# Kernel optimization log

Measured on AMD Instinct MI355X. Metric: run time of the kernel, lower is better.

## Reference

```python
import jax, jax.numpy as jnp
import numpy as np

B, N, D, DEG = 64, 128, 64, 16  # graphs, nodes/graph, emb_dim, degree


def setup_inputs() -> dict:
    key = jax.random.key(0)
    k1, k2 = jax.random.split(key)
    # ring-lattice edges per graph: node i -> (i+k) % N, k=1..DEG (no self loops, no duplicates)
    src_local = jnp.repeat(jnp.arange(N, dtype=jnp.int32), DEG)            # [N*DEG]
    dst_local = (src_local + jnp.tile(jnp.arange(1, DEG + 1, dtype=jnp.int32), N)) % N
    offsets = (jnp.arange(B, dtype=jnp.int32) * N)[:, None]                 # [B,1]
    src = (src_local[None, :] + offsets).reshape(-1)                        # [B*N*DEG]
    dst = (dst_local[None, :] + offsets).reshape(-1)
    edge_index = jnp.stack([src, dst], axis=0)                              # [2, E]
    batch_vec = jnp.repeat(jnp.arange(B, dtype=jnp.int32), N)               # [B*N]
    edge_attr = jax.random.normal(k1, (B * N * DEG, D), dtype=jnp.float32)
    emb_table = jax.random.normal(k2, (3, D), dtype=jnp.float32)
    emb_table = emb_table.at[0].set(0.0)  # padding_idx=0 -> zero row
    return {"edge_attr": edge_attr, "emb_table": emb_table,
            "edge_index": edge_index, "batch_vec": batch_vec,
            "num_graphs": B, "max_nodes": N}


def reference(edge_attr, emb_table, edge_index, batch_vec, num_graphs, max_nodes):
    total_nodes = batch_vec.shape[0]
    ones = jnp.ones((total_nodes,), dtype=jnp.int32)
    counts = jax.ops.segment_sum(ones, batch_vec, num_segments=num_graphs)  # nodes per graph
    offsets = jnp.cumsum(counts) - counts                                   # exclusive cumsum
    local = jnp.arange(total_nodes, dtype=jnp.int32) - offsets[batch_vec]   # node idx within graph

    g = batch_vec[edge_index[0]]            # graph id per edge
    si = local[edge_index[0]]
    di = local[edge_index[1]]

    # to_dense_adj(edge_index, batch, edge_attr): scatter-add edge features -> [B, N, N, D]
    edge_dense = jnp.zeros((num_graphs, max_nodes, max_nodes, edge_attr.shape[-1]),
                           dtype=edge_attr.dtype)
    edge_dense = edge_dense.at[g, si, di].add(edge_attr)

    # A = 2 - dense(edge val 2, self-loop val 1, else 0) -> 0 edge, 1 diag, 2 disconnected/pad
    A = jnp.full((num_graphs, max_nodes, max_nodes), 2, dtype=jnp.int32)
    A = A.at[g, si, di].add(-2)
    A = A.at[batch_vec, local, local].add(-1)

    # Embedding(3, D, padding_idx=0): row 0 is zeros
    emb = emb_table[A] * (A != 0)[..., None].astype(emb_table.dtype)
    return edge_dense + emb
```

## Files before the change

kernel.cpp:

```cpp
#include <hip/hip_runtime.h>


typedef float f4 __attribute__((ext_vector_type(4)));


__global__ __launch_bounds__(256) void fill_u_kernel(
        f4* __restrict__ out, const f4* __restrict__ emb,
        long long total4, int D4, int lg, int lgN) {
    long long base0 = ((long long)blockIdx.x << 11) + threadIdx.x;
    long long stride = (long long)gridDim.x << 11;
    int d4 = (int)base0 & (D4 - 1);
    f4 v1 = emb[D4 + d4];
    f4 v2 = emb[2 * D4 + d4];
    int Nm1 = (1 << lgN) - 1;
    for (long long base = base0; base < total4; base += stride) {
#pragma unroll
        for (int k = 0; k < 8; ++k) {
            long long u = base + (long long)(k << 8);
            long long c = u >> lg;
            int j = (int)c & Nm1;
            int i = (int)(c >> lgN) & Nm1;
            out[u] = (j == i) ? v1 : v2;
        }
    }
}

__global__ __launch_bounds__(256) void edge_u_kernel(
        const f4* __restrict__ attr, const int* __restrict__ eidx,
        f4* __restrict__ out, int E, int N, int D4, int lg) {
    long long idx = (long long)blockIdx.x * 256 + threadIdx.x;
    if (idx < ((long long)E << lg)) {
        int e  = (int)(idx >> lg);
        int d4 = (int)idx & (D4 - 1);
        int s = eidx[e];
        int d = eidx[E + e];
        int dj = d & (N - 1);
        out[(((size_t)s * N + dj) << lg) + d4] = attr[((size_t)e << lg) + d4];
    }
}


__global__ __launch_bounds__(256) void fillprep_kernel(
        f4* __restrict__ out, const f4* __restrict__ emb,
        const int* __restrict__ batch, int* __restrict__ offs,
        int TN, int B, int D4, int fillBlocks) {
    if ((int)blockIdx.x == fillBlocks) {
        __shared__ int cnt[1024];
        for (int i = threadIdx.x; i < B; i += 256) cnt[i] = 0;
        __syncthreads();
        for (int v = threadIdx.x; v < TN; v += 256)
            atomicAdd(&cnt[batch[v]], 1);
        __syncthreads();
        if (threadIdx.x == 0) {
            int acc = 0;
            for (int g = 0; g < B; ++g) { offs[g] = acc; acc += cnt[g]; }
            offs[B] = acc;
        }
        return;
    }
    size_t base = ((size_t)blockIdx.x << 10) + threadIdx.x;
    f4 v2 = emb[2 * D4 + (int)(base & (D4 - 1))];
#pragma unroll
    for (int k = 0; k < 4; ++k)
        out[base + (size_t)k * 256] = v2;
}

__global__ __launch_bounds__(256) void diagedge_kernel(
        const f4* __restrict__ attr, const f4* __restrict__ emb,
        const int* __restrict__ eidx, const int* __restrict__ batch,
        const int* __restrict__ offs, f4* __restrict__ out,
        int E, int N, int TN, int D4, int lg) {
    long long idx = (long long)blockIdx.x * 256 + threadIdx.x;
    long long dUnits = (long long)TN << lg;
    if (idx < dUnits) {
        int n  = (int)(idx >> lg);
        int d4 = (int)idx & (D4 - 1);
        int g = batch[n];
        int i = n - offs[g];
        size_t row = (size_t)(g * N + i);
        out[(row * N + i) * D4 + d4] = emb[D4 + d4];
        return;
    }
    idx -= dUnits;
    if (idx < ((long long)E << lg)) {
        int e  = (int)(idx >> lg);
        int d4 = (int)idx & (D4 - 1);
        int s = eidx[e], d = eidx[E + e];
        int g = batch[s];
        int off = offs[g];
        size_t row = (size_t)(g * N + (s - off));
        out[(row * N + (d - off)) * D4 + d4] = attr[((size_t)e << lg) + d4];
    }
}


__global__ void prep_kernel(const int* __restrict__ batch, int* __restrict__ ws,
                            int TN, int B) {
    extern __shared__ int cnt[];
    for (int i = threadIdx.x; i < B; i += blockDim.x) cnt[i] = 0;
    __syncthreads();
    for (int v = threadIdx.x; v < TN; v += blockDim.x)
        atomicAdd(&cnt[batch[v]], 1);
    __syncthreads();
    if (threadIdx.x == 0) {
        int acc = 0;
        for (int g = 0; g < B; ++g) {
            int c = cnt[g];
            ws[g] = acc; ws[B + g] = c; acc += c;
        }
    }
}

__global__ void fill_kernel(f4* __restrict__ out, const f4* __restrict__ emb,
                            const int* __restrict__ counts, int N, int D4, int jPer) {
    int g  = blockIdx.z;
    int i  = blockIdx.y;
    int d4 = threadIdx.x % D4;
    int jj = threadIdx.x / D4;
    int j  = blockIdx.x * jPer + jj;
    if (j >= N) return;
    f4 v1 = emb[D4 + d4];
    f4 v2 = emb[2 * D4 + d4];
    bool diag = (j == i) && (i < counts[g]);
    f4 v = diag ? v1 : v2;
    size_t row = (size_t)(g * N + i);
    out[(row * N + j) * D4 + d4] = v;
}

__global__ void edge_kernel(const f4* __restrict__ attr, const int* __restrict__ eidx,
                            const int* __restrict__ batch, const int* __restrict__ offs,
                            f4* __restrict__ out, int E, int N, int D4) {
    int idx = blockIdx.x * blockDim.x + threadIdx.x;
    if (idx >= E * D4) return;
    int e  = idx / D4;
    int d4 = idx - e * D4;
    int s  = eidx[e];
    int d  = eidx[E + e];
    int g  = batch[s];
    int off = offs[g];
    out[(((size_t)g * N + (s - off)) * N + (d - off)) * D4 + d4] =
        attr[(size_t)e * D4 + d4];
}

extern "C" void kernel_launch(void* const* d_in, const int* in_sizes, int n_in,
                              void* d_out, int out_size, void* d_ws, size_t ws_size,
                              hipStream_t stream) {
    const float* edge_attr  = (const float*)d_in[0];
    const float* emb_table  = (const float*)d_in[1];
    const int*   edge_index = (const int*)d_in[2];
    const int*   batch_vec  = (const int*)d_in[3];

    int D  = in_sizes[1] / 3;
    int E  = in_sizes[2] / 2;
    int TN = in_sizes[3];
    int D4 = D / 4;
    int N  = (int)((long long)out_size / ((long long)TN * (long long)D));
    int B  = TN / N;

    f4*  out = (f4*)d_out;
    int* ws  = (int*)d_ws;

    auto ispow2 = [](int x) { return x > 0 && (x & (x - 1)) == 0; };
    long long total4 = (long long)out_size / 4;
    bool pow2D4 = ispow2(D4) && D4 <= 256 && (D % 4 == 0);
    int lg = 0; while ((1 << lg) < D4) ++lg;
    int lgN = 0; while ((1 << lgN) < N) ++lgN;

    bool uniform = pow2D4 && ispow2(N) && ((long long)B * N == TN) &&
                   (total4 % 2048 == 0);

    if (uniform) {
        long long chunks = total4 >> 11;
        int fgrid = (int)(chunks < 2048 ? chunks : 2048);
        fill_u_kernel<<<fgrid, 256, 0, stream>>>(out, (const f4*)emb_table,
                                                 total4, D4, lg, lgN);

        long long eUnits = (long long)E << lg;
        int bBlocks = (int)((eUnits + 255) / 256);
        edge_u_kernel<<<bBlocks, 256, 0, stream>>>(
            (const f4*)edge_attr, edge_index, out, E, N, D4, lg);
        return;
    }

    bool fast = pow2D4 && (total4 % 1024 == 0) && B <= 1024 &&
                (long long)ws_size >= (long long)(B + 1) * 4;

    if (fast) {
        int fillBlocks = (int)(total4 >> 10);
        fillprep_kernel<<<fillBlocks + 1, 256, 0, stream>>>(
            out, (const f4*)emb_table, batch_vec, ws, TN, B, D4, fillBlocks);

        long long tUnits = ((long long)TN << lg) + ((long long)E << lg);
        int bBlocks = (int)((tUnits + 255) / 256);
        diagedge_kernel<<<bBlocks, 256, 0, stream>>>(
            (const f4*)edge_attr, (const f4*)emb_table, edge_index, batch_vec,
            ws, out, E, N, TN, D4, lg);
    } else {
        prep_kernel<<<1, 1024, (size_t)B * sizeof(int), stream>>>(batch_vec, ws, TN, B);
        int jPer = 256 / D4; if (jPer < 1) jPer = 1;
        dim3 fgrid((N + jPer - 1) / jPer, N, B);
        fill_kernel<<<fgrid, 256, 0, stream>>>(out, (const f4*)emb_table,
                                               ws + B, N, D4, jPer);
        long long eunits = (long long)E * D4;
        int eblocks = (int)((eunits + 255) / 256);
        edge_kernel<<<eblocks, 256, 0, stream>>>((const f4*)edge_attr, edge_index,
                                                 batch_vec, ws, out, E, N, D4);
    }
}
```

Baseline: 61.36 us.

## Fuse edge scatter into dense fill via precomputed edge-index map

Builds a per-cell edge index map in workspace (init to -1, then scatter edge ids), then writes each output cell once, taking edge attributes when mapped and embedding values otherwise. This removes the second scattered write pass over edge cells. It adds two small kernels and map reads, and it depends on the workspace being large enough.

```diff
diff --git a/kernel.cpp b/kernel.cpp
--- a/kernel.cpp
+++ b/kernel.cpp
@@ -2,6 +2,57 @@
 
 
 typedef float f4 __attribute__((ext_vector_type(4)));
+
+
+__global__ __launch_bounds__(256) void mapinit_kernel(int4* __restrict__ map4,
+                                                      long long n4) {
+    long long idx = (long long)blockIdx.x * 256 + threadIdx.x;
+    long long stride = (long long)gridDim.x * 256;
+    int4 mi = make_int4(-1, -1, -1, -1);
+    for (; idx < n4; idx += stride) map4[idx] = mi;
+}
+
+__global__ __launch_bounds__(256) void mapscat_kernel(const int* __restrict__ eidx,
+                                                      int* __restrict__ map,
+                                                      int E, int N) {
+    int e = blockIdx.x * blockDim.x + threadIdx.x;
+    if (e >= E) return;
+    int s = eidx[e];
+    int d = eidx[E + e];
+    map[(size_t)s * N + (d & (N - 1))] = e;
+}
+
+__global__ __launch_bounds__(256) void fused_u_kernel(
+        const f4* __restrict__ attr, const f4* __restrict__ emb,
+        const int* __restrict__ map, f4* __restrict__ out,
+        long long total4, int D4, int lg, int lgN) {
+    long long base0 = ((long long)blockIdx.x << 11) + threadIdx.x;
+    long long stride = (long long)gridDim.x << 11;
+    int d4 = (int)base0 & (D4 - 1);
+    f4 v1 = emb[D4 + d4];
+    f4 v2 = emb[2 * D4 + d4];
+    int Nm1 = (1 << lgN) - 1;
+    for (long long base = base0; base < total4; base += stride) {
+        int m[8];
+#pragma unroll
+        for (int k = 0; k < 8; ++k)
+            m[k] = map[(base + (long long)(k << 8)) >> lg];
+#pragma unroll
+        for (int k = 0; k < 8; ++k) {
+            long long u = base + (long long)(k << 8);
+            f4 v;
+            if (m[k] >= 0) {
+                v = attr[((size_t)m[k] << lg) + d4];
+            } else {
+                long long c = u >> lg;
+                int j = (int)c & Nm1;
+                int i = (int)(c >> lgN) & Nm1;
+                v = (j == i) ? v1 : v2;
+            }
+            out[u] = v;
+        }
+    }
+}
 
 
 __global__ __launch_bounds__(256) void fill_u_kernel(
@@ -168,13 +219,29 @@
 
     bool uniform = pow2D4 && ispow2(N) && ((long long)B * N == TN) &&
                    (total4 % 2048 == 0);
+    long long cells = (long long)TN * N;
+    bool haveMapWs = (long long)ws_size >= cells * 4 && (cells % 4 == 0);
+
+    if (uniform && haveMapWs) {
+        int* map = ws;
+        long long n4 = cells / 4;
+        int iBlocks = (int)((n4 + 255) / 256); if (iBlocks > 2048) iBlocks = 2048;
+        mapinit_kernel<<<iBlocks, 256, 0, stream>>>((int4*)map, n4);
+        mapscat_kernel<<<(E + 255) / 256, 256, 0, stream>>>(edge_index, map, E, N);
+
+        long long chunks = total4 >> 11;
+        int fgrid = (int)(chunks < 2048 ? chunks : 2048);
+        fused_u_kernel<<<fgrid, 256, 0, stream>>>(
+            (const f4*)edge_attr, (const f4*)emb_table, map, out,
+            total4, D4, lg, lgN);
+        return;
+    }
 
     if (uniform) {
         long long chunks = total4 >> 11;
         int fgrid = (int)(chunks < 2048 ? chunks : 2048);
         fill_u_kernel<<<fgrid, 256, 0, stream>>>(out, (const f4*)emb_table,
                                                  total4, D4, lg, lgN);
-
         long long eUnits = (long long)E << lg;
         int bBlocks = (int)((eUnits + 255) / 256);
         edge_u_kernel<<<bBlocks, 256, 0, stream>>>(
```

New measurement: 81.43 us. +32.7%, slower.
